# Kernel optimization log

Hardware: AMD Instinct MI355X
Metric: run time of the kernel (lower is better)

## Reference

```python
import jax, jax.numpy as jnp
import numpy as np

DIM = 512
NUM_HEADS = 16
HEAD_DIM = DIM // NUM_HEADS
WH, WW = 7, 7
N = WH * WW  # 49 tokens per window
B_ = 4096    # num_windows * batch
TABLE = (2 * WH - 1) * (2 * WW - 1)  # 169


def _make_rel_pos_index():
    # Swin-style relative position index over a Wh x Ww window
    coords_h = np.arange(WH)
    coords_w = np.arange(WW)
    coords = np.stack(np.meshgrid(coords_h, coords_w, indexing='ij'))  # [2, Wh, Ww]
    coords_flat = coords.reshape(2, -1)                                # [2, N]
    rel = coords_flat[:, :, None] - coords_flat[:, None, :]            # [2, N, N]
    rel = rel.transpose(1, 2, 0).astype(np.int32)                      # [N, N, 2]
    rel[:, :, 0] += WH - 1
    rel[:, :, 1] += WW - 1
    rel[:, :, 0] *= 2 * WW - 1
    return rel.sum(-1)  # [N, N] values in [0, TABLE)


def setup_inputs() -> dict:
    key = jax.random.key(0)
    ks = jax.random.split(key, 6)
    s_in = 1.0 / np.sqrt(DIM)
    return {
        'x': jax.random.normal(ks[0], (B_, N, DIM), jnp.float32),
        'qkv_w': jax.random.normal(ks[1], (DIM, 3 * DIM), jnp.float32) * s_in,
        'qkv_b': jnp.zeros((3 * DIM,), jnp.float32),
        'proj_w': jax.random.normal(ks[2], (DIM, DIM), jnp.float32) * s_in,
        'proj_b': jnp.zeros((DIM,), jnp.float32),
        'rel_bias_table': jax.random.normal(ks[3], (TABLE, NUM_HEADS), jnp.float32) * 0.02,
        'rel_pos_index': jnp.asarray(_make_rel_pos_index(), jnp.int32),
    }


def reference(x, qkv_w, qkv_b, proj_w, proj_b, rel_bias_table, rel_pos_index):
    B, n, C = x.shape
    scale = HEAD_DIM ** (-0.5)
    qkv = x @ qkv_w + qkv_b                                   # [B, N, 3C]
    qkv = qkv.reshape(B, n, 3, NUM_HEADS, HEAD_DIM)
    q, k, v = (qkv[:, :, i].transpose(0, 2, 1, 3) for i in range(3))  # [B, H, N, d]
    attn = jnp.einsum('bhnd,bhmd->bhnm', q * scale, k)        # [B, H, N, N]
    # relative position bias gather: [N, N, H] -> [1, H, N, N]
    bias = rel_bias_table[rel_pos_index]                      # [N, N, H]
    attn = attn + bias.transpose(2, 0, 1)[None]
    attn = jax.nn.softmax(attn, axis=-1)
    out = jnp.einsum('bhnm,bhmd->bhnd', attn, v)              # [B, H, N, d]
    out = out.transpose(0, 2, 1, 3).reshape(B, n, C)
    return out @ proj_w + proj_b
```

## Files before the change

kernel.cpp:

```cpp
#include <hip/hip_runtime.h>
#include <hip/hip_bf16.h>
#include <cstdint>
#include <cstdio>

#define M_TOK   200704
#define DIM     512
#define QKV_N   1536
#define NWIN    4096
#define NTOK    49
#define NHEAD   16
#define HD      32
#define TABLE_N 169

typedef float  f32x4  __attribute__((ext_vector_type(4)));
typedef __bf16 bf16x8 __attribute__((ext_vector_type(8)));

__device__ __forceinline__ unsigned short f2bf(float f) {
  union { float f; unsigned u; } v; v.f = f;
  unsigned r = (v.u + 0x7FFFu + ((v.u >> 16) & 1u)) >> 16;
  return (unsigned short)r;
}

__device__ __forceinline__ void gload_lds16(const void* gsrc, void* ldst) {
  __builtin_amdgcn_global_load_lds(
      (const __attribute__((address_space(1))) void*)gsrc,
      (__attribute__((address_space(3))) void*)ldst,
      16, 0, 0);
}

__global__ __launch_bounds__(256) void cast_kernel(
    const float* __restrict__ x, unsigned short* __restrict__ xb)
{
  size_t i = ((size_t)blockIdx.x * 256 + threadIdx.x) * 8;
  float4 a = *(const float4*)(x + i);
  float4 b = *(const float4*)(x + i + 4);
  union { unsigned short s[8]; uint4 v; } pk;
  pk.s[0] = f2bf(a.x); pk.s[1] = f2bf(a.y);
  pk.s[2] = f2bf(a.z); pk.s[3] = f2bf(a.w);
  pk.s[4] = f2bf(b.x); pk.s[5] = f2bf(b.y);
  pk.s[6] = f2bf(b.z); pk.s[7] = f2bf(b.w);
  *(uint4*)(xb + i) = pk.v;
}

__global__ __launch_bounds__(256) void prep_kernel(
    const float* __restrict__ qkv_w, const float* __restrict__ proj_w,
    const float* __restrict__ table, const int* __restrict__ rel_idx,
    unsigned short* __restrict__ Wt, unsigned short* __restrict__ Pt,
    float* __restrict__ biasFull)
{
  int i = blockIdx.x * 256 + threadIdx.x;
  if (i < 786432) {
    int n = i >> 9, k = i & 511;
    Wt[i] = f2bf(qkv_w[(size_t)k * 1536 + n]);
  } else if (i < 786432 + 262144) {
    int j = i - 786432;
    int n = j >> 9, k = j & 511;
    Pt[j] = f2bf(proj_w[(size_t)k * 512 + n]);
  } else if (i < 786432 + 262144 + NHEAD * NTOK * NTOK) {
    int j = i - 1048576;
    int h = j / (NTOK * NTOK), r = j % (NTOK * NTOK);
    biasFull[j] = table[(size_t)rel_idx[r] * NHEAD + h];
  }
}

template<bool CF32>
__global__ __launch_bounds__(256) void gemm_bt(
    const unsigned short* __restrict__ A, const unsigned short* __restrict__ Bt,
    const float* __restrict__ bias, void* __restrict__ Cp,
    int M, int N, int K)
{
  __shared__ unsigned short As[128 * 32];
  __shared__ unsigned short Bs[128 * 32];
  const int tid  = threadIdx.x;
  const int lane = tid & 63;
  const int wave = tid >> 6;
  const int quad = lane >> 4, l16 = lane & 15;
  const int wm = (wave >> 1) * 64, wn = (wave & 1) * 64;

  const unsigned nwg  = gridDim.x * gridDim.y;
  const unsigned flat = blockIdx.y * gridDim.x + blockIdx.x;
  const unsigned cpx  = nwg >> 3;
  const unsigned swz  = (flat & 7u) * cpx + (flat >> 3);
  const size_t n0 = (size_t)(swz % gridDim.x) * 128;
  const size_t m0 = (size_t)(swz / gridDim.x) * 128;

  f32x4 acc[4][4] = {};

  for (int kb = 0; kb < K; kb += 32) {
    #pragma unroll
    for (int p = 0; p < 2; ++p) {
      int c = p * 256 + tid;
      int r = c >> 2, c8 = (c & 3) * 8;
      gload_lds16(A  + (m0 + r) * (size_t)K + kb + c8,
                  &As[(p * 256 + wave * 64) * 8]);
      gload_lds16(Bt + (n0 + r) * (size_t)K + kb + c8,
                  &Bs[(p * 256 + wave * 64) * 8]);
    }
    __syncthreads();

    bf16x8 afr[4], bfr[4];
    #pragma unroll
    for (int mt = 0; mt < 4; ++mt)
      afr[mt] = *(const bf16x8*)(&As[(wm + mt * 16 + l16) * 32 + quad * 8]);
    #pragma unroll
    for (int nt = 0; nt < 4; ++nt)
      bfr[nt] = *(const bf16x8*)(&Bs[(wn + nt * 16 + l16) * 32 + quad * 8]);
    #pragma unroll
    for (int mt = 0; mt < 4; ++mt)
      #pragma unroll
      for (int nt = 0; nt < 4; ++nt)
        acc[mt][nt] = __builtin_amdgcn_mfma_f32_16x16x32_bf16(
            afr[mt], bfr[nt], acc[mt][nt], 0, 0, 0);
    __syncthreads();
  }

  float bcol[4];
  #pragma unroll
  for (int nt = 0; nt < 4; ++nt) bcol[nt] = bias[n0 + wn + nt * 16 + l16];
  float*          Cf = (float*)Cp;
  unsigned short* Ch = (unsigned short*)Cp;
  #pragma unroll
  for (int mt = 0; mt < 4; ++mt)
    #pragma unroll
    for (int r = 0; r < 4; ++r) {
      size_t row = m0 + wm + mt * 16 + quad * 4 + r;
      #pragma unroll
      for (int nt = 0; nt < 4; ++nt) {
        size_t col = n0 + wn + nt * 16 + l16;
        float v = acc[mt][nt][r] + bcol[nt];
        if (CF32) Cf[row * (size_t)N + col] = v;
        else      Ch[row * (size_t)N + col] = f2bf(v);
      }
    }
}

__global__ __launch_bounds__(256) void attn_kernel(
    const unsigned short* __restrict__ qkv,
    const float* __restrict__ biasFull,
    unsigned short* __restrict__ attn_out)
{
  const int b    = blockIdx.x >> 2;
  const int qh   = blockIdx.x & 3;
  const int wave = threadIdx.x >> 6;
  const int h    = qh * 4 + wave;
  const int lane = threadIdx.x & 63;
  const int quad = lane >> 4, l16 = lane & 15;

  __shared__ unsigned short smem[4 * 6144];
  unsigned short* wbase = smem + wave * 6144;
  unsigned short* Qs = wbase;
  unsigned short* Ks = wbase + 2048;
  unsigned short* Vt = wbase + 4096;
  unsigned short* Ps = wbase;

  const size_t rowb = (size_t)b * NTOK;

  #pragma unroll
  for (int seg = 0; seg < 4; ++seg) {
    int t  = seg * 16 + (lane >> 2);
    int c8 = (lane & 3) * 8;
    uint4 zq = {0, 0, 0, 0}, zk = {0, 0, 0, 0}, zv = {0, 0, 0, 0};
    if (t < NTOK) {
      const unsigned short* g = qkv + (rowb + t) * 1536 + h * 32 + c8;
      zq = *(const uint4*)(g);
      zk = *(const uint4*)(g + 512);
      zv = *(const uint4*)(g + 1024);
    }
    *(uint4*)(Qs + t * 32 + c8) = zq;
    *(uint4*)(Ks + t * 32 + c8) = zk;
    union { uint4 v; unsigned short s[8]; } uv; uv.v = zv;
    #pragma unroll
    for (int j = 0; j < 8; ++j) Vt[(c8 + j) * 64 + t] = uv.s[j];
  }

  f32x4 sacc[4][4] = {};
  {
    bf16x8 aq[4], ak[4];
    #pragma unroll
    for (int mt = 0; mt < 4; ++mt)
      aq[mt] = *(const bf16x8*)(Qs + (mt * 16 + l16) * 32 + quad * 8);
    #pragma unroll
    for (int nt = 0; nt < 4; ++nt)
      ak[nt] = *(const bf16x8*)(Ks + (nt * 16 + l16) * 32 + quad * 8);
    #pragma unroll
    for (int mt = 0; mt < 4; ++mt)
      #pragma unroll
      for (int nt = 0; nt < 4; ++nt)
        sacc[mt][nt] = __builtin_amdgcn_mfma_f32_16x16x32_bf16(
            aq[mt], ak[nt], sacc[mt][nt], 0, 0, 0);
  }

  const float scale = 0.17677669529663687f;
  const float* bh = biasFull + h * (NTOK * NTOK);
  #pragma unroll
  for (int mt = 0; mt < 4; ++mt) {
    #pragma unroll
    for (int r = 0; r < 4; ++r) {
      int m = mt * 16 + quad * 4 + r;
      float v[4];
      #pragma unroll
      for (int nt = 0; nt < 4; ++nt) {
        int n = nt * 16 + l16;
        float s = sacc[mt][nt][r] * scale;
        if (m < NTOK && n < NTOK) s += bh[m * NTOK + n];
        v[nt] = (n < NTOK) ? s : -1e30f;
      }
      float mx = fmaxf(fmaxf(v[0], v[1]), fmaxf(v[2], v[3]));
      #pragma unroll
      for (int off = 1; off <= 8; off <<= 1) mx = fmaxf(mx, __shfl_xor(mx, off, 64));
      float e[4], sum = 0.f;
      #pragma unroll
      for (int nt = 0; nt < 4; ++nt) { e[nt] = __expf(v[nt] - mx); sum += e[nt]; }
      #pragma unroll
      for (int off = 1; off <= 8; off <<= 1) sum += __shfl_xor(sum, off, 64);
      float inv = 1.0f / sum;
      #pragma unroll
      for (int nt = 0; nt < 4; ++nt)
        Ps[m * 64 + nt * 16 + l16] = f2bf(e[nt] * inv);
    }
  }

  f32x4 oacc[4][2] = {};
  #pragma unroll
  for (int kt = 0; kt < 2; ++kt) {
    bf16x8 ap[4], av[2];
    #pragma unroll
    for (int mt = 0; mt < 4; ++mt)
      ap[mt] = *(const bf16x8*)(Ps + (mt * 16 + l16) * 64 + kt * 32 + quad * 8);
    #pragma unroll
    for (int dt = 0; dt < 2; ++dt)
      av[dt] = *(const bf16x8*)(Vt + (dt * 16 + l16) * 64 + kt * 32 + quad * 8);
    #pragma unroll
    for (int mt = 0; mt < 4; ++mt)
      #pragma unroll
      for (int dt = 0; dt < 2; ++dt)
        oacc[mt][dt] = __builtin_amdgcn_mfma_f32_16x16x32_bf16(
            ap[mt], av[dt], oacc[mt][dt], 0, 0, 0);
  }

  #pragma unroll
  for (int mt = 0; mt < 4; ++mt)
    #pragma unroll
    for (int r = 0; r < 4; ++r) {
      int m = mt * 16 + quad * 4 + r;
      if (m < NTOK) {
        #pragma unroll
        for (int dt = 0; dt < 2; ++dt)
          attn_out[(rowb + m) * 512 + h * 32 + dt * 16 + l16] =
              f2bf(oacc[mt][dt][r]);
      }
    }
}

#define WS_QKV   0ull
#define WS_ATTN  616562688ull
#define WS_WT    822083584ull
#define WS_PT    823656448ull
#define WS_BIAS  824180736ull
#define WS_END   824334400ull

extern "C" void kernel_launch(void* const* d_in, const int* in_sizes, int n_in,
                              void* d_out, int out_size, void* d_ws, size_t ws_size,
                              hipStream_t stream) {
  const float* x       = (const float*)d_in[0];
  const float* qkv_w   = (const float*)d_in[1];
  const float* qkv_b   = (const float*)d_in[2];
  const float* proj_w  = (const float*)d_in[3];
  const float* proj_b  = (const float*)d_in[4];
  const float* table   = (const float*)d_in[5];
  const int*   rel_idx = (const int*)d_in[6];
  float* out = (float*)d_out;

  if (ws_size < WS_END) {
    fprintf(stderr, "kernel_launch: ws_size %zu < needed %llu\n", ws_size, WS_END);
    return;
  }
  char* ws = (char*)d_ws;
  unsigned short* qkv   = (unsigned short*)(ws + WS_QKV);
  unsigned short* attnb = (unsigned short*)(ws + WS_ATTN);
  unsigned short* xb    = (unsigned short*)(ws + WS_ATTN);
  unsigned short* Wt    = (unsigned short*)(ws + WS_WT);
  unsigned short* Pt    = (unsigned short*)(ws + WS_PT);
  float*          biasF = (float*)(ws + WS_BIAS);

  cast_kernel<<<50176, 256, 0, stream>>>(x, xb);

  prep_kernel<<<4247, 256, 0, stream>>>(qkv_w, proj_w, table, rel_idx, Wt, Pt, biasF);

  dim3 g1(QKV_N / 128, M_TOK / 128);
  gemm_bt<false><<<g1, 256, 0, stream>>>(xb, Wt, qkv_b, qkv, M_TOK, QKV_N, DIM);

  attn_kernel<<<NWIN * 4, 256, 0, stream>>>(qkv, biasF, attnb);

  dim3 g2(DIM / 128, M_TOK / 128);
  gemm_bt<true><<<g2, 256, 0, stream>>>(attnb, Pt, proj_b, out, M_TOK, DIM, DIM);
}
```

Before: 1.676 ms.

## Double-buffer GEMM LDS tiles and shrink attention LDS footprint

The bf16 GEMM now keeps two LDS buffers for the A and B tiles. It issues the global-to-LDS load for the next K slice before running the MFMAs on the current slice, which removes one barrier per iteration and lets loads overlap compute. The attention kernel loads Q fragments straight from global memory into registers and keeps softmax probabilities in the score accumulators. It then writes P to LDS one 32-column half at a time, cutting per-wave LDS from 12KB to 8KB. The cost is double the GEMM's LDS use, extra P-staging traffic inside the kt loop, and uncoalesced direct Q loads.

```diff
diff --git a/kernel.cpp b/kernel.cpp
--- a/kernel.cpp
+++ b/kernel.cpp
@@ -69,8 +69,8 @@
     const float* __restrict__ bias, void* __restrict__ Cp,
     int M, int N, int K)
 {
-  __shared__ unsigned short As[128 * 32];
-  __shared__ unsigned short Bs[128 * 32];
+  __shared__ unsigned short As[2][128 * 32];
+  __shared__ unsigned short Bs[2][128 * 32];
   const int tid  = threadIdx.x;
   const int lane = tid & 63;
   const int wave = tid >> 6;
@@ -86,32 +86,41 @@
 
   f32x4 acc[4][4] = {};
 
-  for (int kb = 0; kb < K; kb += 32) {
+  auto STAGE = [&](int kb, int s) {
     #pragma unroll
     for (int p = 0; p < 2; ++p) {
       int c = p * 256 + tid;
       int r = c >> 2, c8 = (c & 3) * 8;
       gload_lds16(A  + (m0 + r) * (size_t)K + kb + c8,
-                  &As[(p * 256 + wave * 64) * 8]);
+                  &As[s][(p * 256 + wave * 64) * 8]);
       gload_lds16(Bt + (n0 + r) * (size_t)K + kb + c8,
-                  &Bs[(p * 256 + wave * 64) * 8]);
-    }
-    __syncthreads();
+                  &Bs[s][(p * 256 + wave * 64) * 8]);
+    }
+  };
+
+  STAGE(0, 0);
+  __syncthreads();
+
+  int cur = 0;
+  for (int kb = 0; kb < K; kb += 32) {
+    if (kb + 32 < K) STAGE(kb + 32, cur ^ 1);
 
     bf16x8 afr[4], bfr[4];
     #pragma unroll
     for (int mt = 0; mt < 4; ++mt)
-      afr[mt] = *(const bf16x8*)(&As[(wm + mt * 16 + l16) * 32 + quad * 8]);
+      afr[mt] = *(const bf16x8*)(&As[cur][(wm + mt * 16 + l16) * 32 + quad * 8]);
     #pragma unroll
     for (int nt = 0; nt < 4; ++nt)
-      bfr[nt] = *(const bf16x8*)(&Bs[(wn + nt * 16 + l16) * 32 + quad * 8]);
+      bfr[nt] = *(const bf16x8*)(&Bs[cur][(wn + nt * 16 + l16) * 32 + quad * 8]);
     #pragma unroll
     for (int mt = 0; mt < 4; ++mt)
       #pragma unroll
       for (int nt = 0; nt < 4; ++nt)
         acc[mt][nt] = __builtin_amdgcn_mfma_f32_16x16x32_bf16(
             afr[mt], bfr[nt], acc[mt][nt], 0, 0, 0);
+
     __syncthreads();
+    cur ^= 1;
   }
 
   float bcol[4];
@@ -146,11 +155,10 @@
   const int lane = threadIdx.x & 63;
   const int quad = lane >> 4, l16 = lane & 15;
 
-  __shared__ unsigned short smem[4 * 6144];
-  unsigned short* wbase = smem + wave * 6144;
-  unsigned short* Qs = wbase;
-  unsigned short* Ks = wbase + 2048;
-  unsigned short* Vt = wbase + 4096;
+  __shared__ unsigned short smem[4 * 4096];
+  unsigned short* wbase = smem + wave * 4096;
+  unsigned short* Ks = wbase;
+  unsigned short* Vt = wbase + 2048;
   unsigned short* Ps = wbase;
 
   const size_t rowb = (size_t)b * NTOK;
@@ -159,26 +167,29 @@
   for (int seg = 0; seg < 4; ++seg) {
     int t  = seg * 16 + (lane >> 2);
     int c8 = (lane & 3) * 8;
-    uint4 zq = {0, 0, 0, 0}, zk = {0, 0, 0, 0}, zv = {0, 0, 0, 0};
+    uint4 zk = {0, 0, 0, 0}, zv = {0, 0, 0, 0};
     if (t < NTOK) {
       const unsigned short* g = qkv + (rowb + t) * 1536 + h * 32 + c8;
-      zq = *(const uint4*)(g);
       zk = *(const uint4*)(g + 512);
       zv = *(const uint4*)(g + 1024);
     }
-    *(uint4*)(Qs + t * 32 + c8) = zq;
     *(uint4*)(Ks + t * 32 + c8) = zk;
     union { uint4 v; unsigned short s[8]; } uv; uv.v = zv;
     #pragma unroll
     for (int j = 0; j < 8; ++j) Vt[(c8 + j) * 64 + t] = uv.s[j];
   }
 
+  bf16x8 aq[4];
+  #pragma unroll
+  for (int mt = 0; mt < 4; ++mt) {
+    int m = mt * 16 + l16;
+    size_t row = rowb + (m < NTOK ? m : 0);
+    aq[mt] = *(const bf16x8*)(qkv + row * 1536 + h * 32 + quad * 8);
+  }
+
   f32x4 sacc[4][4] = {};
   {
-    bf16x8 aq[4], ak[4];
-    #pragma unroll
-    for (int mt = 0; mt < 4; ++mt)
-      aq[mt] = *(const bf16x8*)(Qs + (mt * 16 + l16) * 32 + quad * 8);
+    bf16x8 ak[4];
     #pragma unroll
     for (int nt = 0; nt < 4; ++nt)
       ak[nt] = *(const bf16x8*)(Ks + (nt * 16 + l16) * 32 + quad * 8);
@@ -215,18 +226,26 @@
       for (int off = 1; off <= 8; off <<= 1) sum += __shfl_xor(sum, off, 64);
       float inv = 1.0f / sum;
       #pragma unroll
-      for (int nt = 0; nt < 4; ++nt)
-        Ps[m * 64 + nt * 16 + l16] = f2bf(e[nt] * inv);
+      for (int nt = 0; nt < 4; ++nt) sacc[mt][nt][r] = e[nt] * inv;
     }
   }
 
   f32x4 oacc[4][2] = {};
   #pragma unroll
   for (int kt = 0; kt < 2; ++kt) {
+    #pragma unroll
+    for (int mt = 0; mt < 4; ++mt)
+      #pragma unroll
+      for (int r = 0; r < 4; ++r) {
+        int m = mt * 16 + quad * 4 + r;
+        #pragma unroll
+        for (int c = 0; c < 2; ++c)
+          Ps[m * 32 + c * 16 + l16] = f2bf(sacc[mt][kt * 2 + c][r]);
+      }
     bf16x8 ap[4], av[2];
     #pragma unroll
     for (int mt = 0; mt < 4; ++mt)
-      ap[mt] = *(const bf16x8*)(Ps + (mt * 16 + l16) * 64 + kt * 32 + quad * 8);
+      ap[mt] = *(const bf16x8*)(Ps + (mt * 16 + l16) * 32 + quad * 8);
     #pragma unroll
     for (int dt = 0; dt < 2; ++dt)
       av[dt] = *(const bf16x8*)(Vt + (dt * 16 + l16) * 64 + kt * 32 + quad * 8);
```

Measured after the change: 1.699 ms. About the same (+1.4%).
